# Performance work log

Hardware: AMD Instinct MI355X
Metric: run time of the kernel (lower is better)

Reference implementation:

```python
import jax, jax.numpy as jnp
import numpy as np

# DNC dims: N memory slots, WM word size, R read heads, H controller hidden, D word_vec
N, WM, R, H, D = 256, 64, 4, 512, 512
T, B = 128, 32
EPS = 1e-6
IFACE = R*WM + R + WM + 1 + WM + WM + R + 1 + 1 + 3*R  # DNC interface vector size


def setup_inputs() -> dict:
    key = jax.random.key(0)
    k = jax.random.split(key, 8)
    in_dim = D + R*WM  # controller sees [x_t ; flattened read vectors]
    w = lambda kk, shape: jax.random.normal(kk, shape, jnp.float32) * 0.02
    return {
        "emb_utt": jax.random.normal(k[0], (T, B, D), jnp.float32),
        "Wx": w(k[1], (in_dim, 4*H)),
        "Wh": w(k[2], (H, 4*H)),
        "b_lstm": jnp.zeros((4*H,), jnp.float32),
        "W_pre": w(k[3], (H, D)),
        "b_pre": jnp.zeros((D,), jnp.float32),
        "W_iface": w(k[4], (H, IFACE)),
        "b_iface": jnp.zeros((IFACE,), jnp.float32),
        "W_rout": w(k[5], (R*WM, D)),
    }


def _content(M, keys, beta):
    # M: (B,N,WM); keys: (B,K,WM); beta: (B,K) -> content weighting (B,K,N)
    Mn = M / jnp.maximum(jnp.linalg.norm(M, axis=-1, keepdims=True), EPS)
    kn = keys / jnp.maximum(jnp.linalg.norm(keys, axis=-1, keepdims=True), EPS)
    sim = jnp.einsum('bkw,bnw->bkn', kn, Mn)
    return jax.nn.softmax(beta[..., None] * sim, axis=-1)


def _allocation(u):
    # usage-sort-based allocation weighting (Graves et al. 2016)
    idx = jnp.argsort(u, axis=1)  # ascending usage
    su = jnp.take_along_axis(u, idx, axis=1)
    excl = jnp.concatenate([jnp.ones_like(su[:, :1]), jnp.cumprod(su, axis=1)[:, :-1]], axis=1)
    a_sorted = (1.0 - su) * excl
    bidx = jnp.arange(u.shape[0])[:, None]
    return jnp.zeros_like(u).at[bidx, idx].set(a_sorted)


def reference(emb_utt, Wx, Wh, b_lstm, W_pre, b_pre, W_iface, b_iface, W_rout):
    Bsz = emb_utt.shape[1]
    eye = jnp.eye(N, dtype=emb_utt.dtype)

    def step(carry, x):
        h, c, M, usage, rw, ww, prec, link, rvec = carry
        # ---- controller (LSTM) ----
        xin = jnp.concatenate([x, rvec.reshape(Bsz, -1)], axis=1)
        gates = xin @ Wx + h @ Wh + b_lstm
        i, f, g, o = jnp.split(gates, 4, axis=1)
        c = jax.nn.sigmoid(f) * c + jax.nn.sigmoid(i) * jnp.tanh(g)
        h = jax.nn.sigmoid(o) * jnp.tanh(c)
        # ---- interface ----
        z = h @ W_iface + b_iface
        off = [0]
        def take(n):
            v = z[:, off[0]:off[0]+n]; off[0] += n; return v
        read_keys = take(R*WM).reshape(Bsz, R, WM)
        read_str = 1.0 + jax.nn.softplus(take(R))
        write_key = take(WM)
        write_str = 1.0 + jax.nn.softplus(take(1))
        erase = jax.nn.sigmoid(take(WM))
        write_vec = take(WM)
        free = jax.nn.sigmoid(take(R))
        alloc_g = jax.nn.sigmoid(take(1))
        write_g = jax.nn.sigmoid(take(1))
        modes = jax.nn.softmax(take(3*R).reshape(Bsz, R, 3), axis=-1)
        # ---- memory write ----
        retention = jnp.prod(1.0 - free[:, :, None] * rw, axis=1)   # (B,N)
        usage = (usage + ww - usage * ww) * retention
        alloc = _allocation(usage)
        cw = _content(M, write_key[:, None, :], write_str)[:, 0, :]  # (B,N)
        ww = write_g * (alloc_g * alloc + (1.0 - alloc_g) * cw)
        M = M * (1.0 - ww[:, :, None] * erase[:, None, :]) + ww[:, :, None] * write_vec[:, None, :]
        # temporal link matrix + precedence
        link = (1.0 - ww[:, :, None] - ww[:, None, :]) * link + ww[:, :, None] * prec[:, None, :]
        link = link * (1.0 - eye)
        prec = (1.0 - jnp.sum(ww, axis=1, keepdims=True)) * prec + ww
        # ---- memory read ----
        cr = _content(M, read_keys, read_str)                        # (B,R,N)
        fw = jnp.einsum('bij,brj->bri', link, rw)                    # forward
        bw = jnp.einsum('bji,brj->bri', link, rw)                    # backward
        rw = modes[..., 0:1] * bw + modes[..., 1:2] * cr + modes[..., 2:3] * fw
        rvec = jnp.einsum('brn,bnw->brw', rw, M)
        out = h @ W_pre + b_pre + rvec.reshape(Bsz, -1) @ W_rout
        return (h, c, M, usage, rw, ww, prec, link, rvec), out

    z = lambda *s: jnp.zeros(s, jnp.float32)
    carry0 = (z(Bsz, H), z(Bsz, H), jnp.full((Bsz, N, WM), EPS, jnp.float32),
              z(Bsz, N), z(Bsz, R, N), z(Bsz, N), z(Bsz, N),
              z(Bsz, N, N), z(Bsz, R, WM))
    _, outs = jax.lax.scan(step, carry0, emb_utt)
    return outs  # (T, B, D)
```

## Files before the change

kernel.cpp:

```cpp
#include <hip/hip_runtime.h>
#include <math.h>

#define TN   256
#define TWM  64
#define TR   4
#define TH   512
#define TD   512
#define TT   128
#define TB   32
#define IFACE 471
#define EPSI 1e-6f

#define OFF_H      0
#define OFF_C      32768
#define OFF_M      49152
#define OFF_USAGE  573440
#define OFF_RW     581632
#define OFF_WW     614400
#define OFF_PRECA  622592
#define OFF_LINK   638976
#define OFF_RVEC   2736128
#define OFF_MNORM  2744320
#define OFF_ZP     2752512
#define OFF_PARSE  2998272
#define OFF_CRS    3012608
#define OFF_FW     3045376
#define OFF_BWP    3078144
#define OFF_CNT    3340288
#define TOTAL_STATE 3341440

#define CNT_ZPG(g) (OFF_CNT + (g)*16)
#define CNT_SB(b)  (OFF_CNT + (8+(b))*16)
#define CNT_FA(b)  (OFF_CNT + (40+(b))*16)

__device__ __forceinline__ float sigm(float x)  { return 1.0f / (1.0f + expf(-x)); }
__device__ __forceinline__ float softpl(float x){ return x > 20.0f ? x : log1pf(expf(x)); }

__device__ __forceinline__ float ldc(const float* p) {
    return __hip_atomic_load(p, __ATOMIC_RELAXED, __HIP_MEMORY_SCOPE_AGENT);
}
__device__ __forceinline__ void stc(float* p, float v) {
    __hip_atomic_store(p, v, __ATOMIC_RELAXED, __HIP_MEMORY_SCOPE_AGENT);
}
__device__ __forceinline__ float4 ldcv4(const float* p) {
    float4 v;
    v.x = ldc(p); v.y = ldc(p + 1); v.z = ldc(p + 2); v.w = ldc(p + 3);
    return v;
}
__device__ __forceinline__ void stcv4(float* p, float4 v) {
    stc(p, v.x); stc(p + 1, v.y); stc(p + 2, v.z); stc(p + 3, v.w);
}

__global__ void k_init(float* ws) {
    int idx = blockIdx.x * 256 + threadIdx.x;
    if (idx >= TOTAL_STATE) return;
    float v = 0.0f;
    if (idx >= OFF_M && idx < OFF_M + TB*TN*TWM) v = EPSI;
    if (idx >= OFF_MNORM && idx < OFF_MNORM + TB*TN) v = 8e-6f;
    ws[idx] = v;
}

__device__ __forceinline__ void out_phase(
    const float* __restrict__ W_pre, const float* __restrict__ b_pre,
    const float* __restrict__ W_rout, const float* __restrict__ ws,
    float* __restrict__ out, float* sm, const int tid, const int B2, const int t)
{
    float* act_s = sm;
    float* red_s = sm + 3072;
    const int q = B2 >> 5, s = (B2 >> 3) & 3, bg = B2 & 7, b0 = bg * 4;
    for (int i = tid; i < 768; i += 512) {
        const int bb = i / 192;
        const int k0 = (i - bb*192) * 4;
        const float* src = (k0 < 512) ? &ws[OFF_H + (t&1)*(TB*TH) + (b0+bb)*TH + k0]
                                      : &ws[OFF_RVEC + (b0+bb)*256 + (k0 - 512)];
        *(float4*)&act_s[bb*768 + k0] = *(const float4*)src;
    }
    __syncthreads();
    const int c0 = q*128 + s*32;
    const int col = tid & 31;
    const int ksb = tid >> 5;
    float a0=0, a1=0, a2=0, a3=0;
    for (int kk = ksb*48; kk < ksb*48 + 48; ++kk) {
        const float w = (kk < 512) ? W_pre[(size_t)kk * 512 + c0 + col]
                                   : W_rout[(size_t)(kk - 512) * 512 + c0 + col];
        a0 += act_s[kk]        * w;
        a1 += act_s[768 + kk]  * w;
        a2 += act_s[1536 + kk] * w;
        a3 += act_s[2304 + kk] * w;
    }
    red_s[(ksb*4 + 0)*32 + col] = a0;
    red_s[(ksb*4 + 1)*32 + col] = a1;
    red_s[(ksb*4 + 2)*32 + col] = a2;
    red_s[(ksb*4 + 3)*32 + col] = a3;
    __syncthreads();
    if (tid < 128) {
        const int cc = tid & 31, bb = tid >> 5;
        float ssum = 0.0f;
        #pragma unroll
        for (int ks2 = 0; ks2 < 16; ++ks2) ssum += red_s[(ks2*4 + bb)*32 + cc];
        ssum += b_pre[c0 + cc];
        out[(size_t)(t - 1) * (TB * TD) + (b0+bb) * TD + c0 + cc] = ssum;
    }
}

__global__ __launch_bounds__(512) void k_front(
    const float* __restrict__ emb, const float* __restrict__ Wx,
    const float* __restrict__ Wh,  const float* __restrict__ b_lstm,
    const float* __restrict__ W_pre, const float* __restrict__ b_pre,
    const float* __restrict__ W_rout,
    float* __restrict__ ws, float* __restrict__ out, int t)
{
    __shared__ __align__(16) float smem[16384];
    const int tid = threadIdx.x;
    if (blockIdx.x >= 128) {
        if (t == 0) return;
        const int raw2 = blockIdx.x - 128;
        const int B2 = (((raw2 >> 2) & 3) << 5) | ((raw2 & 3) << 3) | (raw2 >> 4);
        out_phase(W_pre, b_pre, W_rout, ws, out, smem, tid, B2, t);
        return;
    }
    if (t >= TT) return;

    const int ublk = ((blockIdx.x & 7) << 4) | (blockIdx.x >> 3);
    const int u0  = ublk * 4;
    const int cg  = tid & 3;
    const int bg  = (tid >> 2) & 7;
    const int ks  = tid >> 5;
    const int col0 = cg * 512 + u0;
    const float* hbuf = ws + OFF_H + (t & 1) * (TB * TH);

    float acc[4][4] = {};

    for (int tile = 0; tile < 5; ++tile) {
        const int T0 = tile * 256;
        {
            const int b = tid & 31, kf4 = tid >> 5;
            #pragma unroll
            for (int i = 0; i < 4; ++i) {
                const int kf = kf4 * 4 + i;
                const int kl = kf * 4;
                const int k  = T0 + kl;
                const float* src;
                if (k < 512)      src = emb + (size_t)t * (TB*TD) + b * TD + k;
                else if (k < 768) src = ws + OFF_RVEC + b * 256 + (k - 512);
                else              src = hbuf + b * TH + (k - 768);
                float4 v = *(const float4*)src;
                smem[(kl+0)*32 + b] = v.x;
                smem[(kl+1)*32 + b] = v.y;
                smem[(kl+2)*32 + b] = v.z;
                smem[(kl+3)*32 + b] = v.w;
            }
        }
        __syncthreads();
        {
            const int k0 = T0 + ks * 16;
            const float* wp = (k0 < 768 ? Wx + (size_t)k0 * 2048
                                        : Wh + (size_t)(k0 - 768) * 2048) + col0;
            const float* ap = &smem[(ks * 16) * 32 + bg * 4];
            #pragma unroll 8
            for (int kk = 0; kk < 16; ++kk) {
                float4 wv = *(const float4*)wp; wp += 2048;
                float4 av = *(const float4*)ap; ap += 32;
                acc[0][0] += wv.x*av.x; acc[0][1] += wv.x*av.y; acc[0][2] += wv.x*av.z; acc[0][3] += wv.x*av.w;
                acc[1][0] += wv.y*av.x; acc[1][1] += wv.y*av.y; acc[1][2] += wv.y*av.z; acc[1][3] += wv.y*av.w;
                acc[2][0] += wv.z*av.x; acc[2][1] += wv.z*av.y; acc[2][2] += wv.z*av.z; acc[2][3] += wv.z*av.w;
                acc[3][0] += wv.w*av.x; acc[3][1] += wv.w*av.y; acc[3][2] += wv.w*av.z; acc[3][3] += wv.w*av.w;
            }
        }
        __syncthreads();
    }

    {
        const int rbase = 8192 + ks * 512 + (cg * 8 + bg) * 16;
        *(float4*)&smem[rbase + 0]  = make_float4(acc[0][0], acc[0][1], acc[0][2], acc[0][3]);
        *(float4*)&smem[rbase + 4]  = make_float4(acc[1][0], acc[1][1], acc[1][2], acc[1][3]);
        *(float4*)&smem[rbase + 8]  = make_float4(acc[2][0], acc[2][1], acc[2][2], acc[2][3]);
        *(float4*)&smem[rbase + 12] = make_float4(acc[3][0], acc[3][1], acc[3][2], acc[3][3]);
    }
    __syncthreads();
    {
        const int o = tid;
        float s = 0.0f;
        #pragma unroll
        for (int kq = 0; kq < 16; ++kq) s += smem[8192 + kq * 512 + o];
        const int ocg = o >> 7, obg = (o >> 4) & 7, odu = (o >> 2) & 3, obb = o & 3;
        s += b_lstm[ocg * 512 + u0 + odu];
        smem[(ocg * 4 + odu) * 32 + (obg * 4 + obb)] = s;
    }
    __syncthreads();
    if (tid < 128) {
        const int du = tid >> 5, b = tid & 31;
        const float ig = smem[(0  + du) * 32 + b];
        const float fg = smem[(4  + du) * 32 + b];
        const float gg = smem[(8  + du) * 32 + b];
        const float og = smem[(12 + du) * 32 + b];
        const int ci = b * TH + u0 + du;
        const float cold = ws[OFF_C + ci];
        const float cn = sigm(fg) * cold + sigm(ig) * tanhf(gg);
        const float hn = sigm(og) * tanhf(cn);
        ws[OFF_C + ci] = cn;
        ws[OFF_H + ((t + 1) & 1) * (TB * TH) + ci] = hn;
    }
}

__device__ void stepA_fn(const float* __restrict__ b_if, float* __restrict__ ws,
                         const int t, const int b, const int tid, float* sm)
{
    float* z_s      = sm + 0;
    float* rwf_s    = sm + 480;
    float* ww_old_s = sm + 1504;
    float* ww_s     = sm + 1760;
    float* u_s      = sm + 2016;
    float* prec_s   = sm + 2272;
    float* mnorm_s  = sm + 2528;
    float* alloc_s  = sm + 2784;
    float* cw_s     = sm + 3040;
    float* keysp    = sm + 3296;
    float* wkey_s   = sm + 3552;
    float* erase_s  = sm + 3616;
    float* wvec_s   = sm + 3680;
    float* rstr_s   = sm + 3744;
    float* free_s   = sm + 3748;
    float* modesp   = sm + 3752;
    float* knorm_s  = sm + 3764;
    float* sredA_s  = sm + 3772;
    float* sc_s     = sm + 3780;
    float* Pt_s     = sm + 3788;

    const float* wsM = ws + OFF_M + b * (TN * TWM);
    const float* precOld = ws + OFF_PRECA + (t & 1) * (TB * TN) + b * 256;
    float* precNew = ws + OFF_PRECA + ((t + 1) & 1) * (TB * TN) + b * 256;

    if (tid < 256)       { *(float4*)&rwf_s[tid*4] = *(const float4*)&ws[OFF_RW + b*1024 + tid*4]; }
    else if (tid < 320)  { const int i = tid-256; *(float4*)&ww_old_s[i*4] = *(const float4*)&ws[OFF_WW + b*256 + i*4]; }
    else if (tid < 384)  { const int i = tid-320; *(float4*)&u_s[i*4]      = *(const float4*)&ws[OFF_USAGE + b*256 + i*4]; }
    else if (tid < 448)  { const int i = tid-384; *(float4*)&prec_s[i*4]   = *(const float4*)&precOld[i*4]; }
    else                 { const int i = tid-448; *(float4*)&mnorm_s[i*4]  = *(const float4*)&ws[OFF_MNORM + b*256 + i*4]; }
    if (tid < IFACE) {
        float part[16];
        #pragma unroll
        for (int p = 0; p < 16; ++p)
            part[p] = ldc(&ws[OFF_ZP + ((size_t)p*32 + b) * 480 + tid]);
        float zv = b_if[tid];
        #pragma unroll
        for (int p = 0; p < 16; ++p) zv += part[p];
        z_s[tid] = zv;
    }
    __syncthreads();

    if (tid < IFACE) {
        const float v = z_s[tid];
        if (tid < 256)       keysp[(tid >> 6)*64 + (tid & 63)] = v;
        else if (tid < 260)  rstr_s[tid - 256] = 1.0f + softpl(v);
        else if (tid < 324)  wkey_s[tid - 260] = v;
        else if (tid == 324) sc_s[0] = 1.0f + softpl(v);
        else if (tid < 389)  erase_s[tid - 325] = sigm(v);
        else if (tid < 453)  wvec_s[tid - 389] = v;
        else if (tid < 457)  free_s[tid - 453] = sigm(v);
        else if (tid == 457) sc_s[1] = sigm(v);
        else if (tid == 458) sc_s[2] = sigm(v);
    }
    __syncthreads();
    if (tid < 320) {
        const int w5 = tid >> 6, lane = tid & 63;
        const float v = (w5 == 0) ? wkey_s[lane] : keysp[(w5 - 1)*64 + lane];
        float s = v * v;
        #pragma unroll
        for (int m = 1; m <= 32; m <<= 1) s += __shfl_xor(s, m);
        if (lane == 0) knorm_s[w5] = fmaxf(sqrtf(s), EPSI);
    } else if (tid >= 508) {
        const int r = tid - 508;
        const float m0 = z_s[459 + r*3], m1 = z_s[460 + r*3], m2 = z_s[461 + r*3];
        const float mx = fmaxf(m0, fmaxf(m1, m2));
        const float e0 = expf(m0 - mx), e1 = expf(m1 - mx), e2 = expf(m2 - mx);
        const float s = e0 + e1 + e2;
        modesp[r*3+0] = e0 / s; modesp[r*3+1] = e1 / s; modesp[r*3+2] = e2 / s;
    }
    __syncthreads();

    if (tid < 404) {
        float v;
        if (tid < 256)       v = keysp[tid];
        else if (tid < 320)  v = erase_s[tid - 256];
        else if (tid < 384)  v = wvec_s[tid - 320];
        else if (tid < 388)  v = rstr_s[tid - 384];
        else if (tid < 392)  v = knorm_s[tid - 388 + 1];
        else                 v = modesp[tid - 392];
        stc(&ws[OFF_PARSE + b * 448 + tid], v);
    }
    if (tid < 256) {
        float ret = 1.0f;
        #pragma unroll
        for (int r = 0; r < 4; ++r) ret *= 1.0f - free_s[r] * rwf_s[r*256 + tid];
        const float un = (u_s[tid] + ww_old_s[tid] - u_s[tid] * ww_old_s[tid]) * ret;
        u_s[tid] = un;
        ws[OFF_USAGE + b * 256 + tid] = un;
    }
    __syncthreads();

    {
        const int q = tid >> 8, n = tid & 255;
        const float un = u_s[n];
        float p = 1.0f;
        #pragma unroll 8
        for (int m = q * 128; m < q * 128 + 128; ++m) {
            const float um = u_s[m];
            const bool lt = (um < un) || (um == un && m < n);
            p *= lt ? um : 1.0f;
        }
        Pt_s[q * 256 + n] = p;
    }
    __syncthreads();
    if (tid < 256)
        alloc_s[tid] = (1.0f - u_s[tid]) * Pt_s[tid] * Pt_s[256 + tid];
    __syncthreads();

    {
        const int n = tid >> 1, q2 = tid & 1;
        const float* mp = wsM + n * 64 + q2 * 32;
        float s = 0.0f;
        #pragma unroll
        for (int it = 0; it < 8; ++it) {
            float4 mv = *(const float4*)(mp + it * 4);
            float4 kv = *(const float4*)&wkey_s[q2 * 32 + it * 4];
            s += mv.x*kv.x + mv.y*kv.y + mv.z*kv.z + mv.w*kv.w;
        }
        s += __shfl_xor(s, 1);
        if (q2 == 0) cw_s[n] = sc_s[0] * s / (knorm_s[0] * mnorm_s[n]);
    }
    __syncthreads();
    {
        float v = 0.0f, e = 0.0f;
        if (tid < 256) {
            v = cw_s[tid];
            float m = v;
            #pragma unroll
            for (int mm = 1; mm <= 32; mm <<= 1) m = fmaxf(m, __shfl_xor(m, mm));
            if ((tid & 63) == 0) sredA_s[tid >> 6] = m;
        }
        __syncthreads();
        if (tid == 0) sc_s[4] = fmaxf(fmaxf(sredA_s[0], sredA_s[1]), fmaxf(sredA_s[2], sredA_s[3]));
        __syncthreads();
        if (tid < 256) {
            e = expf(v - sc_s[4]);
            float s2 = e;
            #pragma unroll
            for (int mm = 1; mm <= 32; mm <<= 1) s2 += __shfl_xor(s2, mm);
            if ((tid & 63) == 0) sredA_s[tid >> 6] = s2;
        }
        __syncthreads();
        if (tid == 0) sc_s[5] = sredA_s[0] + sredA_s[1] + sredA_s[2] + sredA_s[3];
        __syncthreads();
        if (tid < 256) cw_s[tid] = e / sc_s[5];
    }
    __syncthreads();

    if (tid < 256) {
        const float wwn = sc_s[2] * (sc_s[1] * alloc_s[tid] + (1.0f - sc_s[1]) * cw_s[tid]);
        ww_s[tid] = wwn;
        stc(&ws[OFF_WW + b * 256 + tid], wwn);
    }
    __syncthreads();
    if (tid < 256) {
        float s = ww_s[tid];
        #pragma unroll
        for (int mm = 1; mm <= 32; mm <<= 1) s += __shfl_xor(s, mm);
        if ((tid & 63) == 0) sredA_s[tid >> 6] = s;
    }
    __syncthreads();
    if (tid == 0) sc_s[3] = sredA_s[0] + sredA_s[1] + sredA_s[2] + sredA_s[3];
    __syncthreads();
    if (tid < 256)
        precNew[tid] = (1.0f - sc_s[3]) * prec_s[tid] + ww_s[tid];
}

__device__ void stepB_fn(float* __restrict__ ws, const int t, const int b,
                         const int tid, float* sm)
{
    float* crp     = sm;
    float* rw2_s   = sm + 1024;
    float* Lt2     = sm + 2048;
    float* md      = sm + 4096;
    float* sredA_s = sm + 4112;
    float* sredB_s = sm + 4120;
    float* gmax_s  = sm + 4128;
    float* gsum_s  = sm + 4132;
    const float* wsM = ws + OFF_M + b * (TN * TWM);

    crp[tid]       = ldc(&ws[OFF_CRS + b*1024 + tid]);
    crp[tid + 512] = ldc(&ws[OFF_CRS + b*1024 + tid + 512]);
    if (tid < 12) md[tid] = ldc(&ws[OFF_PARSE + b*448 + 392 + tid]);
    __syncthreads();

    {
        const int rr = tid >> 8, n = tid & 255, wv = tid >> 6, lane = tid & 63;
        float v0 = crp[rr*256 + n], v1 = crp[(rr + 2)*256 + n];
        float m0 = v0, m1 = v1;
        #pragma unroll
        for (int mm = 1; mm <= 32; mm <<= 1) {
            m0 = fmaxf(m0, __shfl_xor(m0, mm));
            m1 = fmaxf(m1, __shfl_xor(m1, mm));
        }
        if (lane == 0) { sredA_s[wv] = m0; sredB_s[wv] = m1; }
        __syncthreads();
        if (tid < 4) {
            const float* base = (tid & 2) ? sredB_s : sredA_s;
            const int off = (tid & 1) * 4;
            gmax_s[tid] = fmaxf(fmaxf(base[off], base[off+1]), fmaxf(base[off+2], base[off+3]));
        }
        __syncthreads();
        const float e0 = expf(v0 - gmax_s[rr]);
        const float e1 = expf(v1 - gmax_s[rr + 2]);
        float s0 = e0, s1 = e1;
        #pragma unroll
        for (int mm = 1; mm <= 32; mm <<= 1) {
            s0 += __shfl_xor(s0, mm); s1 += __shfl_xor(s1, mm);
        }
        if (lane == 0) { sredA_s[wv] = s0; sredB_s[wv] = s1; }
        __syncthreads();
        if (tid < 4) {
            const float* base = (tid & 2) ? sredB_s : sredA_s;
            const int off = (tid & 1) * 4;
            gsum_s[tid] = base[off] + base[off+1] + base[off+2] + base[off+3];
        }
        __syncthreads();
        crp[rr*256 + n]       = e0 / gsum_s[rr];
        crp[(rr + 2)*256 + n] = e1 / gsum_s[rr + 2];
    }
    __syncthreads();

    {
        const int rr = tid >> 8, n = tid & 255;
        #pragma unroll
        for (int p = 0; p < 2; ++p) {
            const int r = rr + 2 * p;
            float part[8];
            #pragma unroll
            for (int c = 0; c < 8; ++c)
                part[c] = ldc(&ws[OFF_BWP + (size_t)(b*8 + c)*1024 + r*256 + n]);
            const float fwv = ldc(&ws[OFF_FW + b*1024 + r*256 + n]);
            float bw = 0.0f;
            #pragma unroll
            for (int c = 0; c < 8; ++c) bw += part[c];
            const float v = md[r*3] * bw + md[r*3+1] * crp[r*256 + n] + md[r*3+2] * fwv;
            rw2_s[r*256 + n] = v;
            ws[OFF_RW + b*1024 + r*256 + n] = v;
        }
    }
    __syncthreads();

    {
        const int g8 = tid >> 6, w = tid & 63;
        float p0=0, p1=0, p2=0, p3=0;
        const float* mb = wsM + (size_t)(g8 * 32) * 64 + w;
        for (int gg = 0; gg < 4; ++gg) {
            float mv[8];
            #pragma unroll
            for (int j = 0; j < 8; ++j) mv[j] = ldc(mb + (gg*8 + j) * 64);
            #pragma unroll
            for (int j = 0; j < 8; ++j) {
                const int n = g8*32 + gg*8 + j;
                p0 += rw2_s[n]       * mv[j];
                p1 += rw2_s[256 + n] * mv[j];
                p2 += rw2_s[512 + n] * mv[j];
                p3 += rw2_s[768 + n] * mv[j];
            }
        }
        Lt2[(g8*4 + 0)*64 + w] = p0;
        Lt2[(g8*4 + 1)*64 + w] = p1;
        Lt2[(g8*4 + 2)*64 + w] = p2;
        Lt2[(g8*4 + 3)*64 + w] = p3;
    }
    __syncthreads();
    if (tid < 256) {
        const int r = tid >> 6, w = tid & 63;
        float s = 0.0f;
        #pragma unroll
        for (int g = 0; g < 8; ++g) s += Lt2[(g*4 + r)*64 + w];
        ws[OFF_RVEC + b * 256 + tid] = s;
    }
}

__global__ __launch_bounds__(512) void k_step(
    const float* __restrict__ W_if, const float* __restrict__ b_if,
    float* __restrict__ ws, int t)
{
    __shared__ __align__(16) float sm[10272];
    __shared__ int myBatch;
    __shared__ int isTail;
    const int tid = threadIdx.x;
    const int blk = blockIdx.x;

    if (blk < 128) {
        const int bgz = blk >> 4;
        const int q = (blk >> 2) & 3, s = blk & 3;
        const int b0 = bgz * 4;
        float* h1_s = sm;
        if (tid < 128) {
            const int bb = tid >> 5, kk = tid & 31;
            h1_s[bb*32 + kk] = ws[OFF_H + ((t+1)&1)*(TB*TH) + (b0+bb)*TH + q*128 + s*32 + kk];
        }
        __syncthreads();
        if (tid < IFACE) {
            const int col = tid;
            float a0=0, a1=0, a2=0, a3=0;
            const float* wb = W_if + (size_t)(q*128 + s*32) * IFACE + col;
            #pragma unroll 8
            for (int kk = 0; kk < 32; ++kk) {
                const float w = *wb; wb += IFACE;
                a0 += h1_s[kk]      * w;
                a1 += h1_s[32+kk]   * w;
                a2 += h1_s[64+kk]   * w;
                a3 += h1_s[96+kk]   * w;
            }
            const size_t base = OFF_ZP + ((size_t)(q*4+s)*32 + b0) * 480 + col;
            stc(&ws[base],        a0);
            stc(&ws[base + 480],  a1);
            stc(&ws[base + 960],  a2);
            stc(&ws[base + 1440], a3);
        }
        asm volatile("s_waitcnt vmcnt(0)" ::: "memory");
        __syncthreads();
        if (tid == 0) {
            unsigned* cnt = (unsigned*)(ws + CNT_ZPG(bgz));
            const unsigned old = __hip_atomic_fetch_add(cnt, 1u, __ATOMIC_RELAXED, __HIP_MEMORY_SCOPE_AGENT);
            const unsigned base = 16u * (unsigned)t;
            int mb = -1;
            if (old >= base + 12u) {
                mb = b0 + (int)(old - (base + 12u));
                while (__hip_atomic_load(cnt, __ATOMIC_RELAXED, __HIP_MEMORY_SCOPE_AGENT) < base + 16u)
                    __builtin_amdgcn_s_sleep(2);
            }
            myBatch = mb;
        }
        __syncthreads();
        if (myBatch >= 0) {
            stepA_fn(b_if, ws, t, myBatch, tid, sm);
            asm volatile("s_waitcnt vmcnt(0)" ::: "memory");
            __syncthreads();
            if (tid == 0)
                __hip_atomic_store((unsigned*)(ws + CNT_FA(myBatch)), (unsigned)(t + 1),
                                   __ATOMIC_RELAXED, __HIP_MEMORY_SCOPE_AGENT);
        }
    }

    const int b = blk >> 3;
    const int c = blk & 7;
    if (tid == 0) {
        const unsigned* fa = (const unsigned*)(ws + CNT_FA(b));
        while (__hip_atomic_load(fa, __ATOMIC_RELAXED, __HIP_MEMORY_SCOPE_AGENT) < (unsigned)(t + 1))
            __builtin_amdgcn_s_sleep(2);
    }
    __syncthreads();
    asm volatile("" ::: "memory");

    {
        float* ww_s   = sm;
        float* prec_s = sm + 256;
        float* rw_s   = sm + 512;
        float* pk_s   = sm + 1536;
        float* Lt     = sm + 2048;
        const float* precOld = ws + OFF_PRECA + (t & 1) * (TB * TN) + b * 256;

        if (tid < 64)        { *(float4*)&ww_s[tid*4] = ldcv4(&ws[OFF_WW + b*256 + tid*4]); }
        else if (tid < 128)  { const int i = tid-64;  *(float4*)&prec_s[i*4] = *(const float4*)&precOld[i*4]; }
        else if (tid < 384)  { const int i = tid-128; *(float4*)&rw_s[i*4]   = *(const float4*)&ws[OFF_RW + b*1024 + i*4]; }
        else if (tid < 496)  { const int i = tid-384; *(float4*)&pk_s[i*4]   = ldcv4(&ws[OFF_PARSE + b*448 + i*4]); }
        __syncthreads();

        {
            const int ric = tid >> 4, c4 = (tid & 15) * 4;
            const int gi  = c * 32 + ric;
            float* mp = ws + OFF_M + b * (TN*TWM) + gi * 64 + c4;
            float4 m = *(const float4*)mp;
            const float wwi = ww_s[gi];
            float4 er = *(const float4*)&pk_s[256 + c4];
            float4 wv = *(const float4*)&pk_s[320 + c4];
            m.x = m.x * (1.0f - wwi * er.x) + wwi * wv.x;
            m.y = m.y * (1.0f - wwi * er.y) + wwi * wv.y;
            m.z = m.z * (1.0f - wwi * er.z) + wwi * wv.z;
            m.w = m.w * (1.0f - wwi * er.w) + wwi * wv.w;
            stcv4(mp, m);
            float sn = m.x*m.x + m.y*m.y + m.z*m.z + m.w*m.w;
            float d0 = m.x*pk_s[c4]     + m.y*pk_s[c4+1]     + m.z*pk_s[c4+2]     + m.w*pk_s[c4+3];
            float d1 = m.x*pk_s[64+c4]  + m.y*pk_s[64+c4+1]  + m.z*pk_s[64+c4+2]  + m.w*pk_s[64+c4+3];
            float d2 = m.x*pk_s[128+c4] + m.y*pk_s[128+c4+1] + m.z*pk_s[128+c4+2] + m.w*pk_s[128+c4+3];
            float d3 = m.x*pk_s[192+c4] + m.y*pk_s[192+c4+1] + m.z*pk_s[192+c4+2] + m.w*pk_s[192+c4+3];
            #pragma unroll
            for (int mm = 1; mm <= 8; mm <<= 1) {
                sn += __shfl_xor(sn, mm);
                d0 += __shfl_xor(d0, mm); d1 += __shfl_xor(d1, mm);
                d2 += __shfl_xor(d2, mm); d3 += __shfl_xor(d3, mm);
            }
            if ((tid & 15) == 0) {
                const float mn = fmaxf(sqrtf(sn), EPSI);
                ws[OFF_MNORM + b*256 + gi] = mn;
                const float inv = 1.0f / mn;
                stc(&ws[OFF_CRS + b*1024 + 0*256 + gi], pk_s[384+0] * d0 * inv / pk_s[388+0]);
                stc(&ws[OFF_CRS + b*1024 + 1*256 + gi], pk_s[384+1] * d1 * inv / pk_s[388+1]);
                stc(&ws[OFF_CRS + b*1024 + 2*256 + gi], pk_s[384+2] * d2 * inv / pk_s[388+2]);
                stc(&ws[OFF_CRS + b*1024 + 3*256 + gi], pk_s[384+3] * d3 * inv / pk_s[388+3]);
            }
        }

        {
            const int j = tid & 255, p = tid >> 8;
            const float wwj = ww_s[j], pj = prec_s[j];
            #pragma unroll 4
            for (int it = 0; it < 16; ++it) {
                const int ric = it * 2 + p;
                const int gi  = c * 32 + ric;
                float* lp = ws + OFF_LINK + (size_t)b * (TN*TN) + (size_t)gi * 256 + j;
                const float wwi = ww_s[gi];
                float v = (1.0f - wwi - wwj) * (*lp) + wwi * pj;
                if (j == gi) v = 0.0f;
                *lp = v;
                Lt[ric * 257 + j] = v;
            }
        }
        __syncthreads();

        {
            const int ric = tid >> 4, g = tid & 15;
            const int gi = c * 32 + ric;
            float f0=0, f1=0, f2=0, f3=0;
            #pragma unroll 4
            for (int jj = 0; jj < 16; ++jj) {
                const int j = g * 16 + jj;
                const float v = Lt[ric * 257 + j];
                f0 += v * rw_s[j]; f1 += v * rw_s[256+j];
                f2 += v * rw_s[512+j]; f3 += v * rw_s[768+j];
            }
            #pragma unroll
            for (int mm = 1; mm <= 8; mm <<= 1) {
                f0 += __shfl_xor(f0, mm); f1 += __shfl_xor(f1, mm);
                f2 += __shfl_xor(f2, mm); f3 += __shfl_xor(f3, mm);
            }
            if (g == 0) {
                stc(&ws[OFF_FW + b*1024 + gi],       f0);
                stc(&ws[OFF_FW + b*1024 + 256 + gi], f1);
                stc(&ws[OFF_FW + b*1024 + 512 + gi], f2);
                stc(&ws[OFF_FW + b*1024 + 768 + gi], f3);
            }
        }

        {
            const int j = tid & 255, p = tid >> 8;
            float b0=0, b1=0, b2=0, b3=0;
            #pragma unroll 4
            for (int it = 0; it < 16; ++it) {
                const int ric = p * 16 + it;
                const int gi  = c * 32 + ric;
                const float v = Lt[ric * 257 + j];
                b0 += v * rw_s[gi]; b1 += v * rw_s[256+gi];
                b2 += v * rw_s[512+gi]; b3 += v * rw_s[768+gi];
            }
            __syncthreads();
            if (p == 1) { Lt[j] = b0; Lt[256+j] = b1; Lt[512+j] = b2; Lt[768+j] = b3; }
            __syncthreads();
            if (p == 0) {
                stc(&ws[OFF_BWP + (size_t)blk*1024 + j],       b0 + Lt[j]);
                stc(&ws[OFF_BWP + (size_t)blk*1024 + 256 + j], b1 + Lt[256+j]);
                stc(&ws[OFF_BWP + (size_t)blk*1024 + 512 + j], b2 + Lt[512+j]);
                stc(&ws[OFF_BWP + (size_t)blk*1024 + 768 + j], b3 + Lt[768+j]);
            }
        }
    }

    asm volatile("s_waitcnt vmcnt(0)" ::: "memory");
    __syncthreads();
    if (tid == 0) {
        unsigned* cnt = (unsigned*)(ws + CNT_SB(b));
        const unsigned old = __hip_atomic_fetch_add(cnt, 1u, __ATOMIC_RELAXED, __HIP_MEMORY_SCOPE_AGENT);
        isTail = (old == 8u * (unsigned)t + 7u) ? 1 : 0;
    }
    __syncthreads();
    if (!isTail) return;
    stepB_fn(ws, t, b, tid, sm);
}

extern "C" void kernel_launch(void* const* d_in, const int* in_sizes, int n_in,
                              void* d_out, int out_size, void* d_ws, size_t ws_size,
                              hipStream_t stream) {
    const float* emb    = (const float*)d_in[0];
    const float* Wx     = (const float*)d_in[1];
    const float* Wh     = (const float*)d_in[2];
    const float* b_lstm = (const float*)d_in[3];
    const float* W_pre  = (const float*)d_in[4];
    const float* b_pre  = (const float*)d_in[5];
    const float* W_if   = (const float*)d_in[6];
    const float* b_if   = (const float*)d_in[7];
    const float* W_rout = (const float*)d_in[8];
    float* out = (float*)d_out;
    float* ws  = (float*)d_ws;

    k_init<<<(TOTAL_STATE + 255) / 256, 256, 0, stream>>>(ws);
    for (int t = 0; t < TT; ++t) {
        k_front<<<256, 512, 0, stream>>>(emb, Wx, Wh, b_lstm, W_pre, b_pre, W_rout, ws, out, t);
        k_step<<<256, 512, 0, stream>>>(W_if, b_if, ws, t);
    }
    k_front<<<256, 512, 0, stream>>>(emb, Wx, Wh, b_lstm, W_pre, b_pre, W_rout, ws, out, TT);
}
```

Measured before the change: 7.305 ms.

## Fuse LSTM front kernel into step kernel with per-group atomic counters

Merges the LSTM gate kernel (k_front) and the DNC step kernel (k_step) into a single k_all launch per timestep. Blocks publish h via atomic stores and bump a per-group counter, and the interface-projection blocks spin-wait on that counter instead of relying on a kernel boundary. This halves the number of launches per timestep and removes one grid-wide barrier. In exchange it adds spin-wait synchronization and assumes all 256 blocks are co-resident, and the out_phase blocks now share the launch with the step work.

```diff
diff --git a/kernel.cpp b/kernel.cpp
--- a/kernel.cpp
+++ b/kernel.cpp
@@ -27,11 +27,12 @@
 #define OFF_FW     3045376
 #define OFF_BWP    3078144
 #define OFF_CNT    3340288
-#define TOTAL_STATE 3341440
+#define TOTAL_STATE 3341696
 
 #define CNT_ZPG(g) (OFF_CNT + (g)*16)
 #define CNT_SB(b)  (OFF_CNT + (8+(b))*16)
 #define CNT_FA(b)  (OFF_CNT + (40+(b))*16)
+#define CNT_GG(g)  (OFF_CNT + (72+(g))*16)
 
 __device__ __forceinline__ float sigm(float x)  { return 1.0f / (1.0f + expf(-x)); }
 __device__ __forceinline__ float softpl(float x){ return x > 20.0f ? x : log1pf(expf(x)); }
@@ -100,106 +101,6 @@
         for (int ks2 = 0; ks2 < 16; ++ks2) ssum += red_s[(ks2*4 + bb)*32 + cc];
         ssum += b_pre[c0 + cc];
         out[(size_t)(t - 1) * (TB * TD) + (b0+bb) * TD + c0 + cc] = ssum;
-    }
-}
-
-__global__ __launch_bounds__(512) void k_front(
-    const float* __restrict__ emb, const float* __restrict__ Wx,
-    const float* __restrict__ Wh,  const float* __restrict__ b_lstm,
-    const float* __restrict__ W_pre, const float* __restrict__ b_pre,
-    const float* __restrict__ W_rout,
-    float* __restrict__ ws, float* __restrict__ out, int t)
-{
-    __shared__ __align__(16) float smem[16384];
-    const int tid = threadIdx.x;
-    if (blockIdx.x >= 128) {
-        if (t == 0) return;
-        const int raw2 = blockIdx.x - 128;
-        const int B2 = (((raw2 >> 2) & 3) << 5) | ((raw2 & 3) << 3) | (raw2 >> 4);
-        out_phase(W_pre, b_pre, W_rout, ws, out, smem, tid, B2, t);
-        return;
-    }
-    if (t >= TT) return;
-
-    const int ublk = ((blockIdx.x & 7) << 4) | (blockIdx.x >> 3);
-    const int u0  = ublk * 4;
-    const int cg  = tid & 3;
-    const int bg  = (tid >> 2) & 7;
-    const int ks  = tid >> 5;
-    const int col0 = cg * 512 + u0;
-    const float* hbuf = ws + OFF_H + (t & 1) * (TB * TH);
-
-    float acc[4][4] = {};
-
-    for (int tile = 0; tile < 5; ++tile) {
-        const int T0 = tile * 256;
-        {
-            const int b = tid & 31, kf4 = tid >> 5;
-            #pragma unroll
-            for (int i = 0; i < 4; ++i) {
-                const int kf = kf4 * 4 + i;
-                const int kl = kf * 4;
-                const int k  = T0 + kl;
-                const float* src;
-                if (k < 512)      src = emb + (size_t)t * (TB*TD) + b * TD + k;
-                else if (k < 768) src = ws + OFF_RVEC + b * 256 + (k - 512);
-                else              src = hbuf + b * TH + (k - 768);
-                float4 v = *(const float4*)src;
-                smem[(kl+0)*32 + b] = v.x;
-                smem[(kl+1)*32 + b] = v.y;
-                smem[(kl+2)*32 + b] = v.z;
-                smem[(kl+3)*32 + b] = v.w;
-            }
-        }
-        __syncthreads();
-        {
-            const int k0 = T0 + ks * 16;
-            const float* wp = (k0 < 768 ? Wx + (size_t)k0 * 2048
-                                        : Wh + (size_t)(k0 - 768) * 2048) + col0;
-            const float* ap = &smem[(ks * 16) * 32 + bg * 4];
-            #pragma unroll 8
-            for (int kk = 0; kk < 16; ++kk) {
-                float4 wv = *(const float4*)wp; wp += 2048;
-                float4 av = *(const float4*)ap; ap += 32;
-                acc[0][0] += wv.x*av.x; acc[0][1] += wv.x*av.y; acc[0][2] += wv.x*av.z; acc[0][3] += wv.x*av.w;
-                acc[1][0] += wv.y*av.x; acc[1][1] += wv.y*av.y; acc[1][2] += wv.y*av.z; acc[1][3] += wv.y*av.w;
-                acc[2][0] += wv.z*av.x; acc[2][1] += wv.z*av.y; acc[2][2] += wv.z*av.z; acc[2][3] += wv.z*av.w;
-                acc[3][0] += wv.w*av.x; acc[3][1] += wv.w*av.y; acc[3][2] += wv.w*av.z; acc[3][3] += wv.w*av.w;
-            }
-        }
-        __syncthreads();
-    }
-
-    {
-        const int rbase = 8192 + ks * 512 + (cg * 8 + bg) * 16;
-        *(float4*)&smem[rbase + 0]  = make_float4(acc[0][0], acc[0][1], acc[0][2], acc[0][3]);
-        *(float4*)&smem[rbase + 4]  = make_float4(acc[1][0], acc[1][1], acc[1][2], acc[1][3]);
-        *(float4*)&smem[rbase + 8]  = make_float4(acc[2][0], acc[2][1], acc[2][2], acc[2][3]);
-        *(float4*)&smem[rbase + 12] = make_float4(acc[3][0], acc[3][1], acc[3][2], acc[3][3]);
-    }
-    __syncthreads();
-    {
-        const int o = tid;
-        float s = 0.0f;
-        #pragma unroll
-        for (int kq = 0; kq < 16; ++kq) s += smem[8192 + kq * 512 + o];
-        const int ocg = o >> 7, obg = (o >> 4) & 7, odu = (o >> 2) & 3, obb = o & 3;
-        s += b_lstm[ocg * 512 + u0 + odu];
-        smem[(ocg * 4 + odu) * 32 + (obg * 4 + obb)] = s;
-    }
-    __syncthreads();
-    if (tid < 128) {
-        const int du = tid >> 5, b = tid & 31;
-        const float ig = smem[(0  + du) * 32 + b];
-        const float fg = smem[(4  + du) * 32 + b];
-        const float gg = smem[(8  + du) * 32 + b];
-        const float og = smem[(12 + du) * 32 + b];
-        const int ci = b * TH + u0 + du;
-        const float cold = ws[OFF_C + ci];
-        const float cn = sigm(fg) * cold + sigm(ig) * tanhf(gg);
-        const float hn = sigm(og) * tanhf(cn);
-        ws[OFF_C + ci] = cn;
-        ws[OFF_H + ((t + 1) & 1) * (TB * TH) + ci] = hn;
     }
 }
 
@@ -481,43 +382,149 @@
     }
 }
 
-__global__ __launch_bounds__(512) void k_step(
+__global__ __launch_bounds__(512) void k_all(
+    const float* __restrict__ emb, const float* __restrict__ Wx,
+    const float* __restrict__ Wh,  const float* __restrict__ b_lstm,
+    const float* __restrict__ W_pre, const float* __restrict__ b_pre,
+    const float* __restrict__ W_rout,
     const float* __restrict__ W_if, const float* __restrict__ b_if,
-    float* __restrict__ ws, int t)
+    float* __restrict__ ws, float* __restrict__ out, int t)
 {
-    __shared__ __align__(16) float sm[10272];
+    __shared__ __align__(16) float sm[16384];
     __shared__ int myBatch;
     __shared__ int isTail;
     const int tid = threadIdx.x;
     const int blk = blockIdx.x;
 
-    if (blk < 128) {
+    if (blk >= 128) {
+        if (t > 0) {
+            const int raw2 = blk - 128;
+            const int B2 = (((raw2 >> 2) & 3) << 5) | ((raw2 & 3) << 3) | (raw2 >> 4);
+            out_phase(W_pre, b_pre, W_rout, ws, out, sm, tid, B2, t);
+        }
+    } else if (t < TT) {
+        const int ublk = ((blk & 7) << 4) | (blk >> 3);
+        const int u0  = ublk * 4;
+        {
+            const int cg  = tid & 3;
+            const int bg  = (tid >> 2) & 7;
+            const int ks  = tid >> 5;
+            const int col0 = cg * 512 + u0;
+            const float* hbuf = ws + OFF_H + (t & 1) * (TB * TH);
+
+            float acc[4][4] = {};
+
+            for (int tile = 0; tile < 5; ++tile) {
+                const int T0 = tile * 256;
+                {
+                    const int b = tid & 31, kf4 = tid >> 5;
+                    #pragma unroll
+                    for (int i = 0; i < 4; ++i) {
+                        const int kf = kf4 * 4 + i;
+                        const int kl = kf * 4;
+                        const int k  = T0 + kl;
+                        const float* src;
+                        if (k < 512)      src = emb + (size_t)t * (TB*TD) + b * TD + k;
+                        else if (k < 768) src = ws + OFF_RVEC + b * 256 + (k - 512);
+                        else              src = hbuf + b * TH + (k - 768);
+                        float4 v = *(const float4*)src;
+                        sm[(kl+0)*32 + b] = v.x;
+                        sm[(kl+1)*32 + b] = v.y;
+                        sm[(kl+2)*32 + b] = v.z;
+                        sm[(kl+3)*32 + b] = v.w;
+                    }
+                }
+                __syncthreads();
+                {
+                    const int k0 = T0 + ks * 16;
+                    const float* wp = (k0 < 768 ? Wx + (size_t)k0 * 2048
+                                                : Wh + (size_t)(k0 - 768) * 2048) + col0;
+                    const float* ap = &sm[(ks * 16) * 32 + bg * 4];
+                    #pragma unroll 8
+                    for (int kk = 0; kk < 16; ++kk) {
+                        float4 wv = *(const float4*)wp; wp += 2048;
+                        float4 av = *(const float4*)ap; ap += 32;
+                        acc[0][0] += wv.x*av.x; acc[0][1] += wv.x*av.y; acc[0][2] += wv.x*av.z; acc[0][3] += wv.x*av.w;
+                        acc[1][0] += wv.y*av.x; acc[1][1] += wv.y*av.y; acc[1][2] += wv.y*av.z; acc[1][3] += wv.y*av.w;
+                        acc[2][0] += wv.z*av.x; acc[2][1] += wv.z*av.y; acc[2][2] += wv.z*av.z; acc[2][3] += wv.z*av.w;
+                        acc[3][0] += wv.w*av.x; acc[3][1] += wv.w*av.y; acc[3][2] += wv.w*av.z; acc[3][3] += wv.w*av.w;
+                    }
+                }
+                __syncthreads();
+            }
+
+            {
+                const int rbase = 8192 + ks * 512 + (cg * 8 + bg) * 16;
+                *(float4*)&sm[rbase + 0]  = make_float4(acc[0][0], acc[0][1], acc[0][2], acc[0][3]);
+                *(float4*)&sm[rbase + 4]  = make_float4(acc[1][0], acc[1][1], acc[1][2], acc[1][3]);
+                *(float4*)&sm[rbase + 8]  = make_float4(acc[2][0], acc[2][1], acc[2][2], acc[2][3]);
+                *(float4*)&sm[rbase + 12] = make_float4(acc[3][0], acc[3][1], acc[3][2], acc[3][3]);
+            }
+            __syncthreads();
+            {
+                const int o = tid;
+                float s = 0.0f;
+                #pragma unroll
+                for (int kq = 0; kq < 16; ++kq) s += sm[8192 + kq * 512 + o];
+                const int ocg = o >> 7, obg = (o >> 4) & 7, odu = (o >> 2) & 3, obb = o & 3;
+                s += b_lstm[ocg * 512 + u0 + odu];
+                sm[(ocg * 4 + odu) * 32 + (obg * 4 + obb)] = s;
+            }
+            __syncthreads();
+            if (tid < 128) {
+                const int du = tid >> 5, b = tid & 31;
+                const float ig = sm[(0  + du) * 32 + b];
+                const float fg = sm[(4  + du) * 32 + b];
+                const float gg = sm[(8  + du) * 32 + b];
+                const float og = sm[(12 + du) * 32 + b];
+                const int ci = b * TH + u0 + du;
+                const float cold = ws[OFF_C + ci];
+                const float cn = sigm(fg) * cold + sigm(ig) * tanhf(gg);
+                const float hn = sigm(og) * tanhf(cn);
+                ws[OFF_C + ci] = cn;
+                stc(&ws[OFF_H + ((t + 1) & 1) * (TB * TH) + ci], hn);
+            }
+        }
+        asm volatile("s_waitcnt vmcnt(0)" ::: "memory");
+        __syncthreads();
+        if (tid == 0)
+            __hip_atomic_fetch_add((unsigned*)(ws + CNT_GG(ublk >> 3)), 1u,
+                                   __ATOMIC_RELAXED, __HIP_MEMORY_SCOPE_AGENT);
+
         const int bgz = blk >> 4;
         const int q = (blk >> 2) & 3, s = blk & 3;
         const int b0 = bgz * 4;
-        float* h1_s = sm;
-        if (tid < 128) {
-            const int bb = tid >> 5, kk = tid & 31;
-            h1_s[bb*32 + kk] = ws[OFF_H + ((t+1)&1)*(TB*TH) + (b0+bb)*TH + q*128 + s*32 + kk];
-        }
-        __syncthreads();
-        if (tid < IFACE) {
-            const int col = tid;
-            float a0=0, a1=0, a2=0, a3=0;
-            const float* wb = W_if + (size_t)(q*128 + s*32) * IFACE + col;
-            #pragma unroll 8
-            for (int kk = 0; kk < 32; ++kk) {
-                const float w = *wb; wb += IFACE;
-                a0 += h1_s[kk]      * w;
-                a1 += h1_s[32+kk]   * w;
-                a2 += h1_s[64+kk]   * w;
-                a3 += h1_s[96+kk]   * w;
-            }
-            const size_t base = OFF_ZP + ((size_t)(q*4+s)*32 + b0) * 480 + col;
-            stc(&ws[base],        a0);
-            stc(&ws[base + 480],  a1);
-            stc(&ws[base + 960],  a2);
-            stc(&ws[base + 1440], a3);
+        if (tid == 0) {
+            const unsigned* gg = (const unsigned*)(ws + CNT_GG(q*4 + s));
+            while (__hip_atomic_load(gg, __ATOMIC_RELAXED, __HIP_MEMORY_SCOPE_AGENT) < 8u * (unsigned)(t + 1))
+                __builtin_amdgcn_s_sleep(2);
+        }
+        __syncthreads();
+        {
+            float* h1_s = sm;
+            if (tid < 128) {
+                const int bb = tid >> 5, kk = tid & 31;
+                h1_s[bb*32 + kk] = ldc(&ws[OFF_H + ((t+1)&1)*(TB*TH) + (b0+bb)*TH + q*128 + s*32 + kk]);
+            }
+            __syncthreads();
+            if (tid < IFACE) {
+                const int col = tid;
+                float a0=0, a1=0, a2=0, a3=0;
+                const float* wb = W_if + (size_t)(q*128 + s*32) * IFACE + col;
+                #pragma unroll 8
+                for (int kk = 0; kk < 32; ++kk) {
+                    const float w = *wb; wb += IFACE;
+                    a0 += h1_s[kk]      * w;
+                    a1 += h1_s[32+kk]   * w;
+                    a2 += h1_s[64+kk]   * w;
+                    a3 += h1_s[96+kk]   * w;
+                }
+                const size_t base = OFF_ZP + ((size_t)(q*4+s)*32 + b0) * 480 + col;
+                stc(&ws[base],        a0);
+                stc(&ws[base + 480],  a1);
+                stc(&ws[base + 960],  a2);
+                stc(&ws[base + 1440], a3);
+            }
         }
         asm volatile("s_waitcnt vmcnt(0)" ::: "memory");
         __syncthreads();
@@ -543,6 +550,8 @@
                                    __ATOMIC_RELAXED, __HIP_MEMORY_SCOPE_AGENT);
         }
     }
+
+    if (t >= TT) return;
 
     const int b = blk >> 3;
     const int c = blk & 7;
@@ -696,8 +705,9 @@
 
     k_init<<<(TOTAL_STATE + 255) / 256, 256, 0, stream>>>(ws);
     for (int t = 0; t < TT; ++t) {
-        k_front<<<256, 512, 0, stream>>>(emb, Wx, Wh, b_lstm, W_pre, b_pre, W_rout, ws, out, t);
-        k_step<<<256, 512, 0, stream>>>(W_if, b_if, ws, t);
-    }
-    k_front<<<256, 512, 0, stream>>>(emb, Wx, Wh, b_lstm, W_pre, b_pre, W_rout, ws, out, TT);
-}
+        k_all<<<256, 512, 0, stream>>>(emb, Wx, Wh, b_lstm, W_pre, b_pre, W_rout,
+                                       W_if, b_if, ws, out, t);
+    }
+    k_all<<<256, 512, 0, stream>>>(emb, Wx, Wh, b_lstm, W_pre, b_pre, W_rout,
+                                   W_if, b_if, ws, out, TT);
+}
```

After: 7.253 ms. About the same (-0.7%).
